# Performance work log

Hardware: AMD Instinct MI355X
Metric: run time of the kernel (lower is better)

The kernel has to match this reference:

```python
import jax, jax.numpy as jnp
import numpy as np

B, F, V, D = 16384, 16, 100000, 16  # batch, n_fields, vocab, embed_dim; dims = F*D = 256
EPS = 1e-5


def _bn(x, g, b):
    # torch.nn.BatchNorm1d in training mode: biased batch variance
    m = x.mean(0)
    v = x.var(0)
    return g * (x - m) * jax.lax.rsqrt(v + EPS) + b


def setup_inputs() -> dict:
    ks = iter(jax.random.split(jax.random.key(0), 40))

    def rn(shape, s=0.05):
        return jax.random.normal(next(ks), shape, jnp.float32) * s

    return {
        "feat_ids": jax.random.randint(next(ks), (B, F), 0, V, jnp.int32),
        "domain_ids": jax.random.randint(next(ks), (B,), 0, 3, jnp.int32),
        "emb": rn((F, V, D), 0.1),
        "hW0": rn((256, 128)), "hb0": jnp.zeros(128), "hg0": jnp.ones(128), "hbe0": jnp.zeros(128),
        "hW1": rn((128, 64)), "hb1": jnp.zeros(64), "hg1": jnp.ones(64), "hbe1": jnp.zeros(64),
        "hW2": rn((64, 1024)), "hb2": jnp.zeros(1024), "hg2": jnp.ones(1024), "hbe2": jnp.zeros(1024),
        "cw": rn((3, 256)), "cb": jnp.zeros((3, 256)),
        "mW0": rn((256, 512)), "mb0": jnp.zeros(512), "mg0": jnp.ones(512), "mbe0": jnp.zeros(512),
        "mW1": rn((512, 256)), "mb1": jnp.zeros(256), "mg1": jnp.ones(256), "mbe1": jnp.zeros(256),
        "u0": rn((256, 32)), "u1": rn((32, 32)), "v0": rn((32, 32)), "v1": rn((32, 256)),
        "ab0": jnp.zeros(32), "ab1": jnp.zeros(256),
        "gamma1": jnp.ones(256), "bias1": jnp.zeros(256),
        "lw": rn((512,)), "lb": jnp.zeros(1),
    }


def _forward(feat_ids, emb, hW0, hb0, hg0, hbe0, hW1, hb1, hg1, hbe1,
             hW2, hb2, hg2, hbe2, cw, cb, mW0, mb0, mg0, mbe0,
             mW1, mb1, mg1, mbe1, u0, u1, v0, v1, ab0, ab1,
             gamma1, bias1, lw, lb):
    b, f = feat_ids.shape
    # EmbeddingLayer(squeeze_dim=True): per-field lookup then concat -> [B, F*D]
    e = emb[jnp.arange(f)[None, :], feat_ids].reshape(b, -1)
    h = e
    for W, bb, g, be in ((hW0, hb0, hg0, hbe0), (hW1, hb1, hg1, hbe1), (hW2, hb2, hg2, hbe2)):
        h = jax.nn.relu(_bn(h @ W + bb, g, be))
    k = u1.shape[0]
    H = h.reshape(b, k, k)  # [B, k, k]
    # CrossNetwork: x_{l+1} = x0 * (x_l . w_l) + b_l + x_l
    x = e
    for i in range(cw.shape[0]):
        x = e * (x @ cw[i])[:, None] + cb[i] + x
    cn_out = x  # [B, 256]
    m = e
    for W, bb, g, be in ((mW0, mb0, mg0, mbe0), (mW1, mb1, mg1, mbe1)):
        m = jax.nn.relu(_bn(m @ W + bb, g, be))
    # hyper low-rank adapter: einsum('mi,bij,jn->bmn') applied lazily so the
    # [B,256,32] per-sample weight is never materialized (associativity)
    t = jax.nn.sigmoid(jnp.einsum('bi,bij->bj', m @ u0, H) @ v0 + ab0)   # [B, 32]
    t = jnp.einsum('bi,bij->bj', t @ u1, H) @ v1 + ab1                    # [B, 256]
    mu = t.mean(0)
    var = t.var(0, ddof=1)  # torch.var default is unbiased
    m = gamma1 * (t - mu) / jnp.sqrt(var + EPS) + bias1 + m  # norm + residual
    y = jnp.concatenate([cn_out, m], axis=1) @ lw + lb[0]     # LR head
    # Every domain branch computes identical values (shared weights, full-batch
    # input, dropout p=0), so the torch.where domain-select is the identity.
    return jax.nn.sigmoid(y)  # [B]


def reference(feat_ids, domain_ids, emb, hW0, hb0, hg0, hbe0, hW1, hb1, hg1, hbe1,
              hW2, hb2, hg2, hbe2, cw, cb, mW0, mb0, mg0, mbe0,
              mW1, mb1, mg1, mbe1, u0, u1, v0, v1, ab0, ab1,
              gamma1, bias1, lw, lb):
    return _forward(feat_ids, emb, hW0, hb0, hg0, hbe0, hW1, hb1, hg1, hbe1,
                    hW2, hb2, hg2, hbe2, cw, cb, mW0, mb0, mg0, mbe0,
                    mW1, mb1, mg1, mbe1, u0, u1, v0, v1, ab0, ab1,
                    gamma1, bias1, lw, lb)
```

## Files before the change

### kernel.cpp

```cpp
#include <hip/hip_runtime.h>

typedef unsigned short u16;
typedef __attribute__((ext_vector_type(8))) short bf16x8;
typedef __attribute__((ext_vector_type(4))) float f32x4;
#define BATCH 16384

__device__ __forceinline__ float b2f(u16 u){ unsigned int i=((unsigned int)u)<<16; float f; __builtin_memcpy(&f,&i,4); return f; }
__device__ __forceinline__ u16 f2b(float f){ unsigned int x; __builtin_memcpy(&x,&f,4); unsigned int r=(x + 0x7fffu + ((x>>16)&1u))>>16; return (u16)r; }

__global__ __launch_bounds__(256) void prep_kernel(float* __restrict__ S,
                                                   const float* __restrict__ hb0, const float* __restrict__ mb0,
                                                   float* __restrict__ catb,
                                                   const float* __restrict__ w0, const float* __restrict__ w1,
                                                   const float* __restrict__ w2, const float* __restrict__ w3,
                                                   const float* __restrict__ w4, const float* __restrict__ w5,
                                                   const float* __restrict__ w6,
                                                   u16* __restrict__ catWt, u16* __restrict__ t1,
                                                   u16* __restrict__ t2, u16* __restrict__ t4,
                                                   u16* __restrict__ t5, u16* __restrict__ t6,
                                                   const int* __restrict__ ids,
                                                   const float* __restrict__ emb,
                                                   u16* __restrict__ e){
  int blk = blockIdx.x;
  int tid = threadIdx.x;
  if (blk < 18){
    int i = blk*256 + tid;
    if (i < 4480) S[i] = 0.f;
  } else if (blk == 18){
    for (int i = tid; i < 640; i += 256) catb[i] = (i < 128) ? hb0[i] : mb0[i-128];
  } else if (blk < 1523){
    int c = blk - 19;
    if (c < 640){        int idx=c*256+tid;        int n=idx>>8, k=idx&255;
                         catWt[idx] = f2b(n<128 ? w0[k*128+n] : w3[k*512+(n-128)]); }
    else if (c < 672){   int idx=(c-640)*256+tid;  t1[idx]=f2b(w1[(idx%128)*64   + idx/128]); }
    else if (c < 928){   int idx=(c-672)*256+tid;  t2[idx]=f2b(w2[(idx%64)*1024  + idx/64]);  }
    else if (c < 1440){  int idx=(c-928)*256+tid;  t4[idx]=f2b(w4[(idx%512)*256  + idx/512]); }
    else if (c < 1472){  int idx=(c-1440)*256+tid; t5[idx]=f2b(w5[(idx%256)*32   + idx/256]); }
    else {               int idx=(c-1472)*256+tid; t6[idx]=f2b(w6[(idx%32)*256   + idx/32]);  }
  } else {
    int g = blk - 1523;
    int b = g*16 + (tid >> 4), f = tid & 15;
    int id = ids[b*16 + f];
    const float4* src = (const float4*)(emb + ((size_t)f*100000 + (size_t)id)*16);
    float4 v0 = src[0], v1 = src[1], v2 = src[2], v3 = src[3];
    u16 o[16] = { f2b(v0.x),f2b(v0.y),f2b(v0.z),f2b(v0.w), f2b(v1.x),f2b(v1.y),f2b(v1.z),f2b(v1.w),
                  f2b(v2.x),f2b(v2.y),f2b(v2.z),f2b(v2.w), f2b(v3.x),f2b(v3.y),f2b(v3.z),f2b(v3.w) };
    uint4 p0, p1; __builtin_memcpy(&p0, &o[0], 16); __builtin_memcpy(&p1, &o[8], 16);
    uint4* dst = (uint4*)(e + (size_t)b*256 + f*16);
    dst[0] = p0; dst[1] = p1;
  }
}

#define ASTR 40
__global__ __launch_bounds__(256) void gemm_mfma(const u16* __restrict__ A,
                                                 const u16* __restrict__ Wt,
                                                 const float* __restrict__ bias,
                                                 u16* __restrict__ Ca,
                                                 u16* __restrict__ Cb,
                                                 int Nsplit,
                                                 const float* __restrict__ asums,
                                                 const float* __restrict__ asumsq,
                                                 const float* __restrict__ ag,
                                                 const float* __restrict__ abe,
                                                 float* __restrict__ sums,
                                                 float* __restrict__ sumsq,
                                                 int N, int K){
  __shared__ u16 lds[64*ASTR*2];
  __shared__ float bnS[512], bnB[512];
  u16* As = lds;
  u16* Bs = lds + 64*ASTR;
  int tid = threadIdx.x;
  int n0 = blockIdx.x*64, m0 = blockIdx.y*64;
  int srow = tid >> 2, skoff = (tid & 3)*8;
  int lane = tid & 63, w = tid >> 6, quad = lane >> 4, m16 = lane & 15;
  if (asums != nullptr){
    for (int k = tid; k < K; k += 256){
      float mean = asums[k] * (1.f/(float)BATCH);
      float var  = asumsq[k] * (1.f/(float)BATCH) - mean*mean;
      float sc   = ag[k] * rsqrtf(var + 1e-5f);
      bnS[k] = sc;
      bnB[k] = abe[k] - mean*sc;
    }
    __syncthreads();
  }
  f32x4 acc[4] = {};
  int ng = n0 + srow;
  for (int k0 = 0; k0 < K; k0 += 32){
    uint4 av = *(const uint4*)(A + (size_t)(m0+srow)*K + k0 + skoff);
    u16 at[8]; __builtin_memcpy(at, &av, 16);
    if (asums != nullptr){
#pragma unroll
      for (int j=0;j<8;j++){
        float v = b2f(at[j]) * bnS[k0+skoff+j] + bnB[k0+skoff+j];
        at[j] = f2b(v > 0.f ? v : 0.f);
      }
    }
    __builtin_memcpy(&av, at, 16);
    *(uint4*)&As[srow*ASTR + skoff] = av;
    uint4 wv = make_uint4(0u,0u,0u,0u);
    if (ng < N) wv = *(const uint4*)(Wt + (size_t)ng*K + k0 + skoff);
    *(uint4*)&Bs[srow*ASTR + skoff] = wv;
    __syncthreads();
    bf16x8 bfrag = *(bf16x8*)&Bs[(w*16 + m16)*ASTR + quad*8];
#pragma unroll
    for (int mc=0;mc<4;mc++){
      bf16x8 afrag = *(bf16x8*)&As[(mc*16 + m16)*ASTR + quad*8];
      acc[mc] = __builtin_amdgcn_mfma_f32_16x16x32_bf16(afrag, bfrag, acc[mc], 0, 0, 0);
    }
    __syncthreads();
  }
  int cw = n0 + w*16 + m16;
  float bv = (bias != nullptr && cw < N) ? bias[cw] : 0.f;
  float cs = 0.f, cq = 0.f;
  u16* Cs = lds;
#pragma unroll
  for (int mc=0;mc<4;mc++)
#pragma unroll
    for (int r=0;r<4;r++){
      float v = acc[mc][r] + bv;
      cs += v; cq += v*v;
      Cs[(mc*16 + quad*4 + r)*72 + w*16 + m16] = f2b(v);
    }
  if (sums != nullptr){
    cs += __shfl_xor(cs, 16, 64); cs += __shfl_xor(cs, 32, 64);
    cq += __shfl_xor(cq, 16, 64); cq += __shfl_xor(cq, 32, 64);
    if (quad == 0 && cw < N){ atomicAdd(&sums[cw], cs); atomicAdd(&sumsq[cw], cq); }
  }
  __syncthreads();
  int row = tid >> 2, c4 = (tid & 3)*16;
  int cg = n0 + c4;
  if (cg < N){
    u16* outp; int stride, colbase;
    if (Cb != nullptr && n0 >= Nsplit){ outp = Cb; stride = N - Nsplit; colbase = cg - Nsplit; }
    else if (Cb != nullptr){            outp = Ca; stride = Nsplit;     colbase = cg; }
    else {                              outp = Ca; stride = N;          colbase = cg; }
    uint4 p0 = *(uint4*)&Cs[row*72 + c4];
    uint4 p1 = *(uint4*)&Cs[row*72 + c4 + 8];
    *(uint4*)(outp + (size_t)(m0+row)*stride + colbase) = p0;
    *(uint4*)(outp + (size_t)(m0+row)*stride + colbase + 8) = p1;
  }
}

#define HSTR 1056
__global__ __launch_bounds__(256) void adapter_core(const u16* __restrict__ H,
                                                    const u16* __restrict__ Mout,
                                                    const u16* __restrict__ u0t,
                                                    const float* __restrict__ v0,
                                                    const float* __restrict__ u1,
                                                    const float* __restrict__ ab0,
                                                    const float* __restrict__ hsums,
                                                    const float* __restrict__ hsumsq,
                                                    const float* __restrict__ hg,
                                                    const float* __restrict__ hbe,
                                                    const float* __restrict__ msums,
                                                    const float* __restrict__ msumsq,
                                                    const float* __restrict__ mg,
                                                    const float* __restrict__ mbe,
                                                    u16* __restrict__ Z2){
  __shared__ __align__(16) u16 Hs[8*HSTR];
  __shared__ float bnS[1024], bnB[1024];
  __shared__ u16 v0s[1024], u1s[1024];
  __shared__ float mS[256], mB[256];
  __shared__ __align__(16) u16 aS[2048];
  __shared__ float Ps[256], qs[256], t1s[256], ss[256];
  __shared__ float ab0s[32];
  int tid = threadIdx.x;
  int r = tid >> 5, j = tid & 31;
  size_t row0 = (size_t)blockIdx.x * 8;

  for (int k = tid; k < 1024; k += 256){
    float mean = hsums[k] * (1.f/(float)BATCH);
    float var  = hsumsq[k] * (1.f/(float)BATCH) - mean*mean;
    float sc   = hg[k] * rsqrtf(var + 1e-5f);
    bnS[k] = sc; bnB[k] = hbe[k] - mean*sc;
    v0s[k] = f2b(v0[k]); u1s[k] = f2b(u1[k]);
  }
  {
    int c = tid;
    float mean = msums[c] * (1.f/(float)BATCH);
    float var  = msumsq[c] * (1.f/(float)BATCH) - mean*mean;
    float sc   = mg[c] * rsqrtf(var + 1e-5f);
    mS[c] = sc; mB[c] = mbe[c] - mean*sc;
  }
  for (int k = tid; k < 2048; k += 256) aS[k] = Mout[row0*256 + k];
  if (tid < 32) ab0s[tid] = ab0[tid];
  __syncthreads();
  for (int k = tid; k < 2048; k += 256){
    int col = k & 255;
    float v = b2f(aS[k]) * mS[col] + mB[col];
    aS[k] = f2b(v > 0.f ? v : 0.f);
  }
  __syncthreads();
  {
    float acc = 0.f;
    for (int k8 = 0; k8 < 256; k8 += 8){
      uint4 vu = *(const uint4*)(u0t + j*256 + k8);
      uint4 va; __builtin_memcpy(&va, &aS[r*256 + k8], 16);
      u16 ta[8], tu[8]; __builtin_memcpy(ta, &va, 16); __builtin_memcpy(tu, &vu, 16);
#pragma unroll
      for (int q=0;q<8;q++) acc += b2f(ta[q]) * b2f(tu[q]);
    }
    Ps[tid] = acc;
  }
  for (int k = tid; k < 8192; k += 256){
    int rr = k >> 10, col = k & 1023;
    float v = b2f(H[row0*1024 + k]) * bnS[col] + bnB[col];
    Hs[rr*HSTR + col] = f2b(v > 0.f ? v : 0.f);
  }
  __syncthreads();
  float acc = 0.f;
#pragma unroll
  for (int i=0;i<32;i++) acc += Ps[r*32+i] * b2f(Hs[r*HSTR + i*32 + j]);
  qs[tid] = acc;
  __syncthreads();
  acc = ab0s[j];
#pragma unroll
  for (int i=0;i<32;i++) acc += qs[r*32+i] * b2f(v0s[i*32+j]);
  t1s[tid] = 1.f / (1.f + __expf(-acc));
  __syncthreads();
  acc = 0.f;
#pragma unroll
  for (int i=0;i<32;i++) acc += t1s[r*32+i] * b2f(u1s[i*32+j]);
  ss[tid] = acc;
  __syncthreads();
  acc = 0.f;
#pragma unroll
  for (int i=0;i<32;i++) acc += ss[r*32+i] * b2f(Hs[r*HSTR + i*32 + j]);
  Z2[(row0 + r)*32 + j] = f2b(acc);
}

__global__ __launch_bounds__(256) void final_kernel(const u16* __restrict__ e,
                                                    const float* __restrict__ cw,
                                                    const float* __restrict__ cb,
                                                    const u16* __restrict__ t,
                                                    const u16* __restrict__ mo,
                                                    const float* __restrict__ tsums,
                                                    const float* __restrict__ tsumsq,
                                                    const float* __restrict__ tg,
                                                    const float* __restrict__ tbe,
                                                    const float* __restrict__ msums,
                                                    const float* __restrict__ msumsq,
                                                    const float* __restrict__ mg,
                                                    const float* __restrict__ mbe,
                                                    const float* __restrict__ lw,
                                                    const float* __restrict__ lb,
                                                    float* __restrict__ out){
  __shared__ float tS[256], tB[256], mS[256], mB[256];
  int tid = threadIdx.x;
  {
    int c = tid;
    float mean = tsums[c] * (1.f/(float)BATCH);
    float var  = (tsumsq[c] - mean*mean*(float)BATCH) * (1.f/(float)(BATCH-1));
    float sc   = tg[c] * rsqrtf(var + 1e-5f);
    tS[c] = sc; tB[c] = tbe[c] - mean*sc;
    float mmean = msums[c] * (1.f/(float)BATCH);
    float mvar  = msumsq[c] * (1.f/(float)BATCH) - mmean*mmean;
    float msc   = mg[c] * rsqrtf(mvar + 1e-5f);
    mS[c] = msc; mB[c] = mbe[c] - mmean*msc;
  }
  __syncthreads();
  int wave = tid >> 6, lane = tid & 63;
  int b = blockIdx.x*4 + wave;
  int n4 = lane*4;
  ushort4 ev = *(const ushort4*)(e + (size_t)b*256 + n4);
  float ec[4] = { b2f(ev.x), b2f(ev.y), b2f(ev.z), b2f(ev.w) };
  float x[4]  = { ec[0], ec[1], ec[2], ec[3] };
  for (int i=0;i<3;i++){
    float p = 0.f;
#pragma unroll
    for (int q=0;q<4;q++) p += x[q] * cw[i*256 + n4 + q];
#pragma unroll
    for (int o=1;o<64;o<<=1) p += __shfl_xor(p, o, 64);
#pragma unroll
    for (int q=0;q<4;q++) x[q] = ec[q]*p + cb[i*256 + n4 + q] + x[q];
  }
  ushort4 tv = *(const ushort4*)(t  + (size_t)b*256 + n4);
  ushort4 mv = *(const ushort4*)(mo + (size_t)b*256 + n4);
  float ta[4] = { b2f(tv.x), b2f(tv.y), b2f(tv.z), b2f(tv.w) };
  float ma[4] = { b2f(mv.x), b2f(mv.y), b2f(mv.z), b2f(mv.w) };
  float p = 0.f;
#pragma unroll
  for (int q=0;q<4;q++){
    int n = n4 + q;
    p += x[q] * lw[n];
    float mr = ma[q]*mS[n] + mB[n];
    mr = mr > 0.f ? mr : 0.f;
    float mf = tS[n]*ta[q] + tB[n] + mr;
    p += mf * lw[256 + n];
  }
#pragma unroll
  for (int o=32;o>0;o>>=1) p += __shfl_down(p, o, 64);
  if (lane == 0){
    float y = p + lb[0];
    out[b] = 1.f / (1.f + __expf(-y));
  }
}

extern "C" void kernel_launch(void* const* d_in, const int* in_sizes, int n_in,
                              void* d_out, int out_size, void* d_ws, size_t ws_size,
                              hipStream_t stream) {
  const int B = BATCH;
  const int*   feat = (const int*)d_in[0];
  const float* emb  = (const float*)d_in[2];
  const float* hW0 = (const float*)d_in[3],  *hb0 = (const float*)d_in[4],  *hg0 = (const float*)d_in[5],  *hbe0 = (const float*)d_in[6];
  const float* hW1 = (const float*)d_in[7],  *hb1 = (const float*)d_in[8],  *hg1 = (const float*)d_in[9],  *hbe1 = (const float*)d_in[10];
  const float* hW2 = (const float*)d_in[11], *hb2 = (const float*)d_in[12], *hg2 = (const float*)d_in[13], *hbe2 = (const float*)d_in[14];
  const float* cw  = (const float*)d_in[15], *cb  = (const float*)d_in[16];
  const float* mW0 = (const float*)d_in[17], *mb0 = (const float*)d_in[18], *mg0 = (const float*)d_in[19], *mbe0 = (const float*)d_in[20];
  const float* mW1 = (const float*)d_in[21], *mb1 = (const float*)d_in[22], *mg1 = (const float*)d_in[23], *mbe1 = (const float*)d_in[24];
  const float* u0  = (const float*)d_in[25], *u1  = (const float*)d_in[26];
  const float* v0  = (const float*)d_in[27], *v1  = (const float*)d_in[28];
  const float* ab0 = (const float*)d_in[29], *ab1 = (const float*)d_in[30];
  const float* gamma1 = (const float*)d_in[31], *bias1 = (const float*)d_in[32];
  const float* lw  = (const float*)d_in[33], *lb = (const float*)d_in[34];
  float* out = (float*)d_out;

  char* base = (char*)d_ws;
  const size_t MB = 1024*1024;
  u16* H    = (u16*)(base);
  u16* e    = (u16*)(base + 32*MB);
  u16* Y0   = (u16*)(base + 40*MB);
  u16* Y1   = (u16*)(base + 44*MB);
  u16* M0   = (u16*)(base + 48*MB);
  u16* Mout = (u16*)(base + 64*MB);
  u16* T    = (u16*)(base + 72*MB);
  u16* Z2   = (u16*)(base + 80*MB);
  u16* catWt= (u16*)(base + 88*MB);
  u16* hW1t = catWt + 163840;
  u16* hW2t = hW1t + 8192;
  u16* mW1t = hW2t + 65536;
  u16* u0t  = mW1t + 131072;
  u16* v1t  = u0t + 8192;
  float* catb = (float*)(v1t + 8192);
  float* S    = catb + 640;

  prep_kernel<<<2547, 256, 0, stream>>>(S, hb0, mb0, catb,
                                        hW0, hW1, hW2, mW0, mW1, u0, v1,
                                        catWt, hW1t, hW2t, mW1t, u0t, v1t,
                                        feat, emb, e);

  gemm_mfma<<<dim3(10, B/64), 256, 0, stream>>>(e, catWt, catb, Y0, M0, 128,
      nullptr, nullptr, nullptr, nullptr, S+0, S+640, 640, 256);

  gemm_mfma<<<dim3(1, B/64), 256, 0, stream>>>(Y0, hW1t, hb1, Y1, nullptr, 0,
      S+0, S+640, hg0, hbe0, S+1280, S+1344, 64, 128);
  gemm_mfma<<<dim3(16, B/64), 256, 0, stream>>>(Y1, hW2t, hb2, H, nullptr, 0,
      S+1280, S+1344, hg1, hbe1, S+1408, S+2432, 1024, 64);

  gemm_mfma<<<dim3(4, B/64), 256, 0, stream>>>(M0, mW1t, mb1, Mout, nullptr, 0,
      S+128, S+768, mg0, mbe0, S+3456, S+3712, 256, 512);

  adapter_core<<<B/8, 256, 0, stream>>>(H, Mout, u0t, v0, u1, ab0,
      S+1408, S+2432, hg2, hbe2, S+3456, S+3712, mg1, mbe1, Z2);
  gemm_mfma<<<dim3(4, B/64), 256, 0, stream>>>(Z2, v1t, ab1, T, nullptr, 0,
      nullptr, nullptr, nullptr, nullptr, S+3968, S+4224, 256, 32);

  final_kernel<<<B/4, 256, 0, stream>>>(e, cw, cb, T, Mout,
      S+3968, S+4224, gamma1, bias1,
      S+3456, S+3712, mg1, mbe1, lw, lb, out);
}
```

Measured before the change: 360.9 us.

## Add 128x128-tile MFMA GEMM kernel and use it for wide layers

Adds a new GEMM kernel that uses 128x128 output tiles, with each wave computing a 4x4 grid of 16x16 MFMA tiles, replacing the 64x64 kernel for the concatenated first layer, the hyper-net third layer, the main second layer and the adapter output projection. The larger tile raises arithmetic intensity per LDS load and halves global re-reads of A and W. In exchange it uses more registers and launches fewer blocks, which can lower occupancy. The old kernel loses its split-output option and stays in use only for the N=64 layer.

```diff
diff --git a/kernel.cpp b/kernel.cpp
--- a/kernel.cpp
+++ b/kernel.cpp
@@ -51,13 +51,143 @@
   }
 }
 
+#define LSTRD 40
+__global__ __launch_bounds__(256) void gemm128(const u16* __restrict__ A,
+                                               const u16* __restrict__ Wt,
+                                               const float* __restrict__ bias,
+                                               u16* __restrict__ Ca,
+                                               u16* __restrict__ Cb,
+                                               int Nsplit,
+                                               const float* __restrict__ asums,
+                                               const float* __restrict__ asumsq,
+                                               const float* __restrict__ ag,
+                                               const float* __restrict__ abe,
+                                               float* __restrict__ sums,
+                                               float* __restrict__ sumsq,
+                                               int N, int K){
+  __shared__ u16 lds[128*LSTRD*2];
+  __shared__ float bnS[512], bnB[512];
+  u16* As = lds;
+  u16* Bs = lds + 128*LSTRD;
+  int tid = threadIdx.x;
+  int n0 = blockIdx.x*128, m0 = blockIdx.y*128;
+  int lane = tid & 63, w = tid >> 6, quad = lane >> 4, l16 = lane & 15;
+  int wm = w >> 1, wn = w & 1;
+  if (asums != nullptr){
+    for (int k = tid; k < K; k += 256){
+      float mean = asums[k] * (1.f/(float)BATCH);
+      float var  = asumsq[k] * (1.f/(float)BATCH) - mean*mean;
+      float sc   = ag[k] * rsqrtf(var + 1e-5f);
+      bnS[k] = sc;
+      bnB[k] = abe[k] - mean*sc;
+    }
+    __syncthreads();
+  }
+  f32x4 acc[4][4] = {};
+  int srow = tid >> 1, soff = (tid & 1)*16;
+  for (int k0 = 0; k0 < K; k0 += 32){
+    const u16* ap = A + (size_t)(m0+srow)*K + k0 + soff;
+    uint4 av0 = *(const uint4*)ap;
+    uint4 av1 = *(const uint4*)(ap + 8);
+    if (asums != nullptr){
+      u16 at[16]; __builtin_memcpy(at, &av0, 16); __builtin_memcpy(at+8, &av1, 16);
+#pragma unroll
+      for (int j=0;j<16;j++){
+        float v = b2f(at[j]) * bnS[k0+soff+j] + bnB[k0+soff+j];
+        at[j] = f2b(v > 0.f ? v : 0.f);
+      }
+      __builtin_memcpy(&av0, at, 16); __builtin_memcpy(&av1, at+8, 16);
+    }
+    *(uint4*)&As[srow*LSTRD + soff] = av0;
+    *(uint4*)&As[srow*LSTRD + soff + 8] = av1;
+    const u16* bp = Wt + (size_t)(n0+srow)*K + k0 + soff;
+    uint4 bv0 = *(const uint4*)bp;
+    uint4 bv1 = *(const uint4*)(bp + 8);
+    *(uint4*)&Bs[srow*LSTRD + soff] = bv0;
+    *(uint4*)&Bs[srow*LSTRD + soff + 8] = bv1;
+    __syncthreads();
+    bf16x8 af[4], bf[4];
+#pragma unroll
+    for (int mt=0;mt<4;mt++) af[mt] = *(bf16x8*)&As[(wm*64 + mt*16 + l16)*LSTRD + quad*8];
+#pragma unroll
+    for (int nt=0;nt<4;nt++) bf[nt] = *(bf16x8*)&Bs[(wn*64 + nt*16 + l16)*LSTRD + quad*8];
+#pragma unroll
+    for (int mt=0;mt<4;mt++)
+#pragma unroll
+      for (int nt=0;nt<4;nt++)
+        acc[mt][nt] = __builtin_amdgcn_mfma_f32_16x16x32_bf16(af[mt], bf[nt], acc[mt][nt], 0, 0, 0);
+    __syncthreads();
+  }
+  float bv[4];
+#pragma unroll
+  for (int nt=0;nt<4;nt++){
+    int col = n0 + wn*64 + nt*16 + l16;
+    bv[nt] = (bias != nullptr) ? bias[col] : 0.f;
+  }
+  float cs[4] = {0,0,0,0}, cq[4] = {0,0,0,0};
+#pragma unroll
+  for (int mt=0;mt<4;mt++)
+#pragma unroll
+    for (int nt=0;nt<4;nt++)
+#pragma unroll
+      for (int r=0;r<4;r++){
+        float v = acc[mt][nt][r] + bv[nt];
+        acc[mt][nt][r] = v;
+        cs[nt] += v; cq[nt] += v*v;
+      }
+  if (sums != nullptr){
+#pragma unroll
+    for (int nt=0;nt<4;nt++){
+      cs[nt] += __shfl_xor(cs[nt], 16, 64); cs[nt] += __shfl_xor(cs[nt], 32, 64);
+      cq[nt] += __shfl_xor(cq[nt], 16, 64); cq[nt] += __shfl_xor(cq[nt], 32, 64);
+    }
+    if (quad == 0){
+#pragma unroll
+      for (int nt=0;nt<4;nt++){
+        int col = n0 + wn*64 + nt*16 + l16;
+        atomicAdd(&sums[col], cs[nt]); atomicAdd(&sumsq[col], cq[nt]);
+      }
+    }
+  }
+  u16* outp; int stride, cb0;
+  if (Cb != nullptr && n0 >= Nsplit){ outp = Cb; stride = N - Nsplit; cb0 = n0 - Nsplit; }
+  else if (Cb != nullptr){            outp = Ca; stride = Nsplit;     cb0 = n0; }
+  else {                              outp = Ca; stride = N;          cb0 = n0; }
+  u16* Cs = lds;
+#pragma unroll
+  for (int half=0; half<2; half++){
+    if (wm == half){
+#pragma unroll
+      for (int mt=0;mt<4;mt++)
+#pragma unroll
+        for (int nt=0;nt<4;nt++)
+#pragma unroll
+          for (int r=0;r<4;r++)
+            Cs[(mt*16 + quad*4 + r)*136 + wn*64 + nt*16 + l16] = f2b(acc[mt][nt][r]);
+    }
+    __syncthreads();
+    {
+      int row = tid >> 2, cseg = (tid & 3)*32;
+      u16* dst = outp + (size_t)(m0 + half*64 + row)*stride + cb0 + cseg;
+      const u16* src = &Cs[row*136 + cseg];
+      uint4 p0 = *(const uint4*)(src);
+      uint4 p1 = *(const uint4*)(src + 8);
+      uint4 p2 = *(const uint4*)(src + 16);
+      uint4 p3 = *(const uint4*)(src + 24);
+      *(uint4*)(dst)      = p0;
+      *(uint4*)(dst + 8)  = p1;
+      *(uint4*)(dst + 16) = p2;
+      *(uint4*)(dst + 24) = p3;
+    }
+    __syncthreads();
+  }
+}
+
 #define ASTR 40
 __global__ __launch_bounds__(256) void gemm_mfma(const u16* __restrict__ A,
                                                  const u16* __restrict__ Wt,
                                                  const float* __restrict__ bias,
-                                                 u16* __restrict__ Ca,
-                                                 u16* __restrict__ Cb,
-                                                 int Nsplit,
+                                                 u16* __restrict__ C,
                                                  const float* __restrict__ asums,
                                                  const float* __restrict__ asumsq,
                                                  const float* __restrict__ ag,
@@ -110,14 +240,14 @@
     __syncthreads();
   }
   int cw = n0 + w*16 + m16;
-  float bv = (bias != nullptr && cw < N) ? bias[cw] : 0.f;
+  float bvv = (bias != nullptr && cw < N) ? bias[cw] : 0.f;
   float cs = 0.f, cq = 0.f;
   u16* Cs = lds;
 #pragma unroll
   for (int mc=0;mc<4;mc++)
 #pragma unroll
     for (int r=0;r<4;r++){
-      float v = acc[mc][r] + bv;
+      float v = acc[mc][r] + bvv;
       cs += v; cq += v*v;
       Cs[(mc*16 + quad*4 + r)*72 + w*16 + m16] = f2b(v);
     }
@@ -130,14 +260,10 @@
   int row = tid >> 2, c4 = (tid & 3)*16;
   int cg = n0 + c4;
   if (cg < N){
-    u16* outp; int stride, colbase;
-    if (Cb != nullptr && n0 >= Nsplit){ outp = Cb; stride = N - Nsplit; colbase = cg - Nsplit; }
-    else if (Cb != nullptr){            outp = Ca; stride = Nsplit;     colbase = cg; }
-    else {                              outp = Ca; stride = N;          colbase = cg; }
     uint4 p0 = *(uint4*)&Cs[row*72 + c4];
     uint4 p1 = *(uint4*)&Cs[row*72 + c4 + 8];
-    *(uint4*)(outp + (size_t)(m0+row)*stride + colbase) = p0;
-    *(uint4*)(outp + (size_t)(m0+row)*stride + colbase + 8) = p1;
+    *(uint4*)(C + (size_t)(m0+row)*N + cg) = p0;
+    *(uint4*)(C + (size_t)(m0+row)*N + cg + 8) = p1;
   }
 }
 
@@ -339,20 +465,20 @@
                                         catWt, hW1t, hW2t, mW1t, u0t, v1t,
                                         feat, emb, e);
 
-  gemm_mfma<<<dim3(10, B/64), 256, 0, stream>>>(e, catWt, catb, Y0, M0, 128,
+  gemm128<<<dim3(5, B/128), 256, 0, stream>>>(e, catWt, catb, Y0, M0, 128,
       nullptr, nullptr, nullptr, nullptr, S+0, S+640, 640, 256);
 
-  gemm_mfma<<<dim3(1, B/64), 256, 0, stream>>>(Y0, hW1t, hb1, Y1, nullptr, 0,
+  gemm_mfma<<<dim3(1, B/64), 256, 0, stream>>>(Y0, hW1t, hb1, Y1,
       S+0, S+640, hg0, hbe0, S+1280, S+1344, 64, 128);
-  gemm_mfma<<<dim3(16, B/64), 256, 0, stream>>>(Y1, hW2t, hb2, H, nullptr, 0,
+  gemm128<<<dim3(8, B/128), 256, 0, stream>>>(Y1, hW2t, hb2, H, nullptr, 0,
       S+1280, S+1344, hg1, hbe1, S+1408, S+2432, 1024, 64);
 
-  gemm_mfma<<<dim3(4, B/64), 256, 0, stream>>>(M0, mW1t, mb1, Mout, nullptr, 0,
+  gemm128<<<dim3(2, B/128), 256, 0, stream>>>(M0, mW1t, mb1, Mout, nullptr, 0,
       S+128, S+768, mg0, mbe0, S+3456, S+3712, 256, 512);
 
   adapter_core<<<B/8, 256, 0, stream>>>(H, Mout, u0t, v0, u1, ab0,
       S+1408, S+2432, hg2, hbe2, S+3456, S+3712, mg1, mbe1, Z2);
-  gemm_mfma<<<dim3(4, B/64), 256, 0, stream>>>(Z2, v1t, ab1, T, nullptr, 0,
+  gemm128<<<dim3(2, B/128), 256, 0, stream>>>(Z2, v1t, ab1, T, nullptr, 0,
       nullptr, nullptr, nullptr, nullptr, S+3968, S+4224, 256, 32);
 
   final_kernel<<<B/4, 256, 0, stream>>>(e, cw, cb, T, Mout,
```

Result: slower. 384.8 us (+6.6%).

## Template GEMM on K-tile size and prefetch next tile into registers

Applied to the files above, without the earlier changes.

The MFMA GEMM kernel is templated on the K-tile depth (64 for most calls, 32 for the K=32 one), so each thread loads 16 elements per step and the block runs two MFMA sub-steps per barrier pair. It also software-prefetches the next A/B tile into registers before the barrier, so global loads overlap with the MFMA work. The aim is to halve the number of sync iterations and hide load latency, at the cost of more registers and a larger LDS tile.

```diff
diff --git a/kernel.cpp b/kernel.cpp
--- a/kernel.cpp
+++ b/kernel.cpp
@@ -51,7 +51,7 @@
   }
 }
 
-#define ASTR 40
+template<int BK>
 __global__ __launch_bounds__(256) void gemm_mfma(const u16* __restrict__ A,
                                                  const u16* __restrict__ Wt,
                                                  const float* __restrict__ bias,
@@ -65,14 +65,16 @@
                                                  float* __restrict__ sums,
                                                  float* __restrict__ sumsq,
                                                  int N, int K){
-  __shared__ u16 lds[64*ASTR*2];
+  constexpr int STR = BK + 8;
+  constexpr int EPT = BK/4;
+  __shared__ u16 lds[64*STR*2];
   __shared__ float bnS[512], bnB[512];
   u16* As = lds;
-  u16* Bs = lds + 64*ASTR;
+  u16* Bs = lds + 64*STR;
   int tid = threadIdx.x;
   int n0 = blockIdx.x*64, m0 = blockIdx.y*64;
-  int srow = tid >> 2, skoff = (tid & 3)*8;
   int lane = tid & 63, w = tid >> 6, quad = lane >> 4, m16 = lane & 15;
+  int srow = tid >> 2, skoff = (tid & 3)*EPT;
   if (asums != nullptr){
     for (int k = tid; k < K; k += 256){
       float mean = asums[k] * (1.f/(float)BATCH);
@@ -85,39 +87,65 @@
   }
   f32x4 acc[4] = {};
   int ng = n0 + srow;
-  for (int k0 = 0; k0 < K; k0 += 32){
-    uint4 av = *(const uint4*)(A + (size_t)(m0+srow)*K + k0 + skoff);
-    u16 at[8]; __builtin_memcpy(at, &av, 16);
+  uint4 a0, a1, b0, b1;
+  {
+    const u16* ap = A + (size_t)(m0+srow)*K + skoff;
+    a0 = *(const uint4*)ap;
+    if (EPT == 16) a1 = *(const uint4*)(ap + 8);
+    if (ng < N){
+      const u16* bp = Wt + (size_t)ng*K + skoff;
+      b0 = *(const uint4*)bp;
+      if (EPT == 16) b1 = *(const uint4*)(bp + 8);
+    } else { b0 = make_uint4(0u,0u,0u,0u); b1 = b0; }
+  }
+  for (int k0 = 0; k0 < K; k0 += BK){
+    u16 at[EPT];
+    __builtin_memcpy(at, &a0, 16);
+    if (EPT == 16) __builtin_memcpy(at+8, &a1, 16);
     if (asums != nullptr){
 #pragma unroll
-      for (int j=0;j<8;j++){
+      for (int j=0;j<EPT;j++){
         float v = b2f(at[j]) * bnS[k0+skoff+j] + bnB[k0+skoff+j];
         at[j] = f2b(v > 0.f ? v : 0.f);
       }
     }
-    __builtin_memcpy(&av, at, 16);
-    *(uint4*)&As[srow*ASTR + skoff] = av;
-    uint4 wv = make_uint4(0u,0u,0u,0u);
-    if (ng < N) wv = *(const uint4*)(Wt + (size_t)ng*K + k0 + skoff);
-    *(uint4*)&Bs[srow*ASTR + skoff] = wv;
+    uint4 s0, s1;
+    __builtin_memcpy(&s0, at, 16);
+    *(uint4*)&As[srow*STR + skoff] = s0;
+    if (EPT == 16){ __builtin_memcpy(&s1, at+8, 16); *(uint4*)&As[srow*STR + skoff + 8] = s1; }
+    *(uint4*)&Bs[srow*STR + skoff] = b0;
+    if (EPT == 16) *(uint4*)&Bs[srow*STR + skoff + 8] = b1;
+    if (k0 + BK < K){
+      const u16* ap = A + (size_t)(m0+srow)*K + k0 + BK + skoff;
+      a0 = *(const uint4*)ap;
+      if (EPT == 16) a1 = *(const uint4*)(ap + 8);
+      if (ng < N){
+        const u16* bp = Wt + (size_t)ng*K + k0 + BK + skoff;
+        b0 = *(const uint4*)bp;
+        if (EPT == 16) b1 = *(const uint4*)(bp + 8);
+      }
+    }
     __syncthreads();
-    bf16x8 bfrag = *(bf16x8*)&Bs[(w*16 + m16)*ASTR + quad*8];
-#pragma unroll
-    for (int mc=0;mc<4;mc++){
-      bf16x8 afrag = *(bf16x8*)&As[(mc*16 + m16)*ASTR + quad*8];
-      acc[mc] = __builtin_amdgcn_mfma_f32_16x16x32_bf16(afrag, bfrag, acc[mc], 0, 0, 0);
+#pragma unroll
+    for (int sub=0; sub<BK/32; sub++){
+      bf16x8 bfrag = *(bf16x8*)&Bs[(w*16 + m16)*STR + sub*32 + quad*8];
+#pragma unroll
+      for (int mc=0;mc<4;mc++){
+        bf16x8 afrag = *(bf16x8*)&As[(mc*16 + m16)*STR + sub*32 + quad*8];
+        acc[mc] = __builtin_amdgcn_mfma_f32_16x16x32_bf16(afrag, bfrag, acc[mc], 0, 0, 0);
+      }
     }
     __syncthreads();
   }
   int cw = n0 + w*16 + m16;
-  float bv = (bias != nullptr && cw < N) ? bias[cw] : 0.f;
+  float bvv = (bias != nullptr && cw < N) ? bias[cw] : 0.f;
   float cs = 0.f, cq = 0.f;
   u16* Cs = lds;
 #pragma unroll
   for (int mc=0;mc<4;mc++)
 #pragma unroll
     for (int r=0;r<4;r++){
-      float v = acc[mc][r] + bv;
+      float v = acc[mc][r] + bvv;
       cs += v; cq += v*v;
       Cs[(mc*16 + quad*4 + r)*72 + w*16 + m16] = f2b(v);
     }
@@ -339,20 +367,20 @@
                                         catWt, hW1t, hW2t, mW1t, u0t, v1t,
                                         feat, emb, e);
 
-  gemm_mfma<<<dim3(10, B/64), 256, 0, stream>>>(e, catWt, catb, Y0, M0, 128,
+  gemm_mfma<64><<<dim3(10, B/64), 256, 0, stream>>>(e, catWt, catb, Y0, M0, 128,
       nullptr, nullptr, nullptr, nullptr, S+0, S+640, 640, 256);
 
-  gemm_mfma<<<dim3(1, B/64), 256, 0, stream>>>(Y0, hW1t, hb1, Y1, nullptr, 0,
+  gemm_mfma<64><<<dim3(1, B/64), 256, 0, stream>>>(Y0, hW1t, hb1, Y1, nullptr, 0,
       S+0, S+640, hg0, hbe0, S+1280, S+1344, 64, 128);
-  gemm_mfma<<<dim3(16, B/64), 256, 0, stream>>>(Y1, hW2t, hb2, H, nullptr, 0,
+  gemm_mfma<64><<<dim3(16, B/64), 256, 0, stream>>>(Y1, hW2t, hb2, H, nullptr, 0,
       S+1280, S+1344, hg1, hbe1, S+1408, S+2432, 1024, 64);
 
-  gemm_mfma<<<dim3(4, B/64), 256, 0, stream>>>(M0, mW1t, mb1, Mout, nullptr, 0,
+  gemm_mfma<64><<<dim3(4, B/64), 256, 0, stream>>>(M0, mW1t, mb1, Mout, nullptr, 0,
       S+128, S+768, mg0, mbe0, S+3456, S+3712, 256, 512);
 
   adapter_core<<<B/8, 256, 0, stream>>>(H, Mout, u0t, v0, u1, ab0,
       S+1408, S+2432, hg2, hbe2, S+3456, S+3712, mg1, mbe1, Z2);
-  gemm_mfma<<<dim3(4, B/64), 256, 0, stream>>>(Z2, v1t, ab1, T, nullptr, 0,
+  gemm_mfma<32><<<dim3(4, B/64), 256, 0, stream>>>(Z2, v1t, ab1, T, nullptr, 0,
       nullptr, nullptr, nullptr, nullptr, S+3968, S+4224, 256, 32);
 
   final_kernel<<<B/4, 256, 0, stream>>>(e, cw, cb, T, Mout,
```

Measured after the change: 344.7 us. 4.5% less time.
